# Performance work log

Hardware: AMD Instinct MI355X
Metric: run time of the kernel (lower is better)

## Reference

```python
import jax, jax.numpy as jnp
import numpy as np

B, N, D, E = 2, 50000, 128, 640000


def setup_inputs() -> dict:
    key = jax.random.key(0)
    ks = jax.random.split(key, 7)
    x = jax.random.normal(ks[0], (B, N, D), dtype=jnp.float32)
    edge_index = jax.random.randint(ks[1], (2, E), 0, N)
    edge_attr = jax.random.uniform(ks[2], (E,), dtype=jnp.float32)
    s = 1.0 / np.sqrt(D)
    W1 = jax.random.uniform(ks[3], (D, D), jnp.float32, -s, s)
    b1 = jax.random.uniform(ks[4], (D,), jnp.float32, -s, s)
    W2 = jax.random.uniform(ks[5], (D, D), jnp.float32, -s, s)
    b2 = jax.random.uniform(ks[6], (D,), jnp.float32, -s, s)
    return {"x": x, "edge_index": edge_index, "edge_attr": edge_attr,
            "W1": W1, "b1": b1, "W2": W2, "b2": b2}


def _gcn_layer(x, W, b, row, col, norm, n):
    # x: [B, N, D] -> transform then gather-scale-scatter along edges
    h = jnp.einsum('bnd,df->bnf', x, W)
    msg = h[:, row, :] * norm[None, :, None]          # [B, E2, D]
    agg = jax.vmap(lambda m: jax.ops.segment_sum(m, col, num_segments=n))(msg)
    return agg + b


def reference(x, edge_index, edge_attr, W1, b1, W2, b2):
    n = x.shape[1]
    row, col = edge_index[0], edge_index[1]
    # GCNConv default: add self loops (weight 1), symmetric normalization
    loop = jnp.arange(n)
    row2 = jnp.concatenate([row, loop])
    col2 = jnp.concatenate([col, loop])
    w2 = jnp.concatenate([edge_attr, jnp.ones((n,), edge_attr.dtype)])
    deg = jax.ops.segment_sum(w2, col2, num_segments=n)
    dinv = jnp.where(deg > 0, jax.lax.rsqrt(deg), 0.0)
    norm = dinv[row2] * w2 * dinv[col2]               # [E2]
    # dropout is identity in eval mode
    h = jax.nn.relu(_gcn_layer(x, W1, b1, row2, col2, norm, n))
    h = jax.nn.relu(_gcn_layer(h, W2, b2, row2, col2, norm, n))
    return h
```

## Files before the change

### kernel.cpp

```cpp
#include <hip/hip_runtime.h>

#define NNODES 50000
#define NBATCH 2
#define DIM    128
#define NEDGE  640000
#define M_TOT  (NBATCH*NNODES)
#define NXCD   8
#define NBL_N  196

typedef unsigned short u16;
typedef unsigned int   u32;
typedef unsigned long long u64;

typedef __attribute__((ext_vector_type(8))) short bf16x8;
typedef __attribute__((ext_vector_type(4))) float f32x4;

__device__ __forceinline__ float bf2f(u16 u){ return __uint_as_float(((u32)u)<<16); }
__device__ __forceinline__ u16 f2bf(float f){
    u32 x = __float_as_uint(f);
    x += 0x7fffu + ((x>>16)&1u);
    return (u16)(x>>16);
}

__global__ __launch_bounds__(256) void count_k(const int* __restrict__ ei,
                                               const float* __restrict__ ea,
                                               u64* __restrict__ part,
                                               u32* __restrict__ rankpack){
    u32 xcc = __builtin_amdgcn_s_getreg(6164) & 7u;
    int e = blockIdx.x*256 + threadIdx.x;
    if (e < NEDGE){
        int c = ei[NEDGE + e];
        u64 inc = (((u64)__float2uint_rn(ea[e] * 16777216.0f)) << 32) | 1ull;
        u64 old = __hip_atomic_fetch_add(&part[(size_t)xcc*NNODES + c], inc,
                                         __ATOMIC_RELAXED, __HIP_MEMORY_SCOPE_WORKGROUP);
        rankpack[e] = ((u32)old & 0xffffu) | (xcc << 16);
    }
}

__global__ __launch_bounds__(256) void scan1(const u64* __restrict__ part,
                                             int* __restrict__ cnt,
                                             int* __restrict__ poff,
                                             float* __restrict__ dinv,
                                             int* colstart, int* bsum){
    __shared__ int s[256];
    int tid = threadIdx.x;
    int n = blockIdx.x*256 + tid;
    int v = 0;
    if (n < NNODES){
        int run = 0; u64 fsum = 0;
        #pragma unroll
        for (int p = 0; p < NXCD; ++p){
            u64 pv = part[(size_t)p*NNODES + n];
            poff[p*NNODES + n] = run;
            run  += (int)(pv & 0xffffffffu);
            fsum += (pv >> 32);
        }
        cnt[n] = run;
        v = run;
        float deg = 1.0f + (float)fsum * (1.0f/16777216.0f);
        dinv[n] = rsqrtf(deg);
    }
    s[tid] = v; __syncthreads();
    #pragma unroll
    for (int off = 1; off < 256; off <<= 1){
        int t = (tid >= off) ? s[tid-off] : 0;
        __syncthreads();
        s[tid] += t;
        __syncthreads();
    }
    if (n < NNODES) colstart[n] = s[tid] - v;
    if (tid == 255) bsum[blockIdx.x] = s[255];
}

__global__ __launch_bounds__(256) void fill_k(const int* __restrict__ ei,
                                              const float* __restrict__ ea,
                                              const float* __restrict__ dinv,
                                              const int* __restrict__ colstart,
                                              const int* __restrict__ bsum,
                                              const int* __restrict__ poff,
                                              const u32* __restrict__ rankpack,
                                              int* __restrict__ colstartF,
                                              u32* __restrict__ epk){
    __shared__ int s[256];
    __shared__ int pre[256];
    int tid = threadIdx.x;
    int v = (tid < NBL_N) ? bsum[tid] : 0;
    s[tid] = v; __syncthreads();
    #pragma unroll
    for (int off = 1; off < 256; off <<= 1){
        int t = (tid >= off) ? s[tid-off] : 0;
        __syncthreads();
        s[tid] += t;
        __syncthreads();
    }
    pre[tid] = s[tid] - v;
    __syncthreads();

    int e = blockIdx.x*256 + tid;
    if (e < NEDGE){
        int r = ei[e], c = ei[NEDGE + e];
        u32 rp = rankpack[e];
        int base = colstart[c] + pre[c >> 8];
        colstartF[c] = base;
        int pos = base + poff[(rp >> 16)*NNODES + c] + (int)(rp & 0xffffu);
        float w = dinv[r] * ea[e] * dinv[c];
        epk[pos] = (u32)r | ((u32)f2bf(w) << 16);
    }
}

__global__ __launch_bounds__(256) void transposeW(const float* __restrict__ W1, u16* __restrict__ Wt1,
                                                  const float* __restrict__ W2, u16* __restrict__ Wt2,
                                                  u64* __restrict__ part){
    int i = blockIdx.x*256 + threadIdx.x;
    const float* W = (i < 16384) ? W1 : W2;
    u16* Wt       = (i < 16384) ? Wt1 : Wt2;
    int ii = i & 16383;
    int k = ii >> 7, n = ii & 127;
    Wt[n*DIM + k] = f2bf(W[ii]);
    for (int z = i; z < NXCD*NNODES; z += 32768) part[z] = 0;
}

__device__ __forceinline__ bf16x8 load_frag(const float* A, size_t off){
    const f32x4* ap = (const f32x4*)(A + off);
    f32x4 lo = __builtin_nontemporal_load(ap);
    f32x4 hi = __builtin_nontemporal_load(ap + 1);
    bf16x8 r;
    r[0] = (short)f2bf(lo.x); r[1] = (short)f2bf(lo.y);
    r[2] = (short)f2bf(lo.z); r[3] = (short)f2bf(lo.w);
    r[4] = (short)f2bf(hi.x); r[5] = (short)f2bf(hi.y);
    r[6] = (short)f2bf(hi.z); r[7] = (short)f2bf(hi.w);
    return r;
}
__device__ __forceinline__ bf16x8 load_frag(const u16* A, size_t off){
    return *(const bf16x8*)(A + off);
}

template <typename AT, bool PERM>
__global__ __launch_bounds__(256, 4) void gemm128(const AT* __restrict__ A,
                                                  const u16* __restrict__ Wt,
                                                  u16* __restrict__ H, int M){
    __shared__ u16 Wl[128][136];
    int tid = threadIdx.x;
    {
        const uint4* src = (const uint4*)Wt;
        #pragma unroll
        for (int j = 0; j < 8; ++j){
            int g = tid + j*256;
            *(uint4*)&Wl[g >> 4][(g & 15)*8] = src[g];
        }
    }
    __syncthreads();

    int wave = tid >> 6, lane = tid & 63;
    int quad = lane >> 4, r = lane & 15;
    int row0 = blockIdx.x*128;
    int rbase = row0 + wave*32;

    f32x4 acc[2][8];
    #pragma unroll
    for (int mt = 0; mt < 2; ++mt)
        #pragma unroll
        for (int nt = 0; nt < 8; ++nt)
            acc[mt][nt] = (f32x4){0.f,0.f,0.f,0.f};

    #pragma unroll
    for (int ks = 0; ks < 4; ++ks){
        bf16x8 af[2];
        #pragma unroll
        for (int mt = 0; mt < 2; ++mt){
            int row = rbase + mt*16 + r;
            if (row < M)
                af[mt] = load_frag(A, (size_t)row*DIM + ks*32 + quad*8);
            else
                af[mt] = (bf16x8){0,0,0,0,0,0,0,0};
        }
        #pragma unroll
        for (int nt = 0; nt < 8; ++nt){
            bf16x8 bfr = *(const bf16x8*)&Wl[nt*16 + r][ks*32 + quad*8];
            #pragma unroll
            for (int mt = 0; mt < 2; ++mt)
                acc[mt][nt] = __builtin_amdgcn_mfma_f32_16x16x32_bf16(af[mt], bfr, acc[mt][nt], 0, 0, 0);
        }
    }

    __syncthreads();
    #pragma unroll
    for (int mt = 0; mt < 2; ++mt)
        #pragma unroll
        for (int nt = 0; nt < 8; ++nt)
            #pragma unroll
            for (int reg = 0; reg < 4; ++reg)
                Wl[wave*32 + mt*16 + quad*4 + reg][nt*16 + r] = f2bf(acc[mt][nt][reg]);
    __syncthreads();

    #pragma unroll
    for (int j = 0; j < 8; ++j){
        int g = tid + j*256;
        int rl = g >> 4, ch = g & 15;
        int row = row0 + rl;
        if (row < M){
            size_t hrow;
            if (PERM){
                int b = (row >= NNODES);
                hrow = (size_t)(2*(row - b*NNODES) + b);
            } else {
                hrow = (size_t)row;
            }
            *(uint4*)((char*)H + hrow*256 + ch*16) = *(const uint4*)&Wl[rl][ch*8];
        }
    }
}

template <bool OUT_F32>
__global__ __launch_bounds__(256) void gather6_k(const u16* __restrict__ Hi,
                                                 const u32* __restrict__ epk,
                                                 const int* __restrict__ colstartF,
                                                 const int* __restrict__ cnt,
                                                 const float* __restrict__ dinv,
                                                 const float* __restrict__ bias,
                                                 void* __restrict__ out){
    int wave = threadIdx.x >> 6, lane = threadIdx.x & 63;
    int n = blockIdx.x*4 + wave;
    if (n >= NNODES) return;
    const char* Hb = (const char*)Hi;

    float a0, a1, a2, a3;
    {
        uint2 sv = *(const uint2*)(Hb + (size_t)n*512 + lane*8);
        float dn = dinv[n], dn2 = dn*dn;
        a0 = dn2*__uint_as_float(sv.x << 16);
        a1 = dn2*__uint_as_float(sv.x & 0xffff0000u);
        a2 = dn2*__uint_as_float(sv.y << 16);
        a3 = dn2*__uint_as_float(sv.y & 0xffff0000u);
    }

    int s = colstartF[n], c = cnt[n];
    for (int base = 0; base < c; base += 64){
        int m = min(64, c - base);
        u32 em = 0;
        if (lane < m) em = epk[s + base + lane];
        for (int j = 0; j < m; j += 8){
            #pragma unroll
            for (int g = 0; g < 8; ++g){
                u32 me = __shfl(em, j + g);
                uint2 v = *(const uint2*)(Hb + (size_t)(me & 0xffffu)*512 + lane*8);
                float w = __uint_as_float(me & 0xffff0000u);
                a0 = fmaf(w, __uint_as_float(v.x << 16), a0);
                a1 = fmaf(w, __uint_as_float(v.x & 0xffff0000u), a1);
                a2 = fmaf(w, __uint_as_float(v.y << 16), a2);
                a3 = fmaf(w, __uint_as_float(v.y & 0xffff0000u), a3);
            }
        }
    }

    int sub = lane & 31, b = lane >> 5;
    float4 bb = ((const float4*)bias)[sub];
    a0 = fmaxf(a0 + bb.x, 0.f);
    a1 = fmaxf(a1 + bb.y, 0.f);
    a2 = fmaxf(a2 + bb.z, 0.f);
    a3 = fmaxf(a3 + bb.w, 0.f);
    if (OUT_F32){
        float* O = (float*)out + ((size_t)b*NNODES + n)*DIM + sub*4;
        *(float4*)O = make_float4(a0, a1, a2, a3);
    } else {
        char* O = (char*)out + (size_t)n*512 + lane*8;
        uint2 pk;
        pk.x = (u32)f2bf(a0) | ((u32)f2bf(a1) << 16);
        pk.y = (u32)f2bf(a2) | ((u32)f2bf(a3) << 16);
        *(uint2*)O = pk;
    }
}

extern "C" void kernel_launch(void* const* d_in, const int* in_sizes, int n_in,
                              void* d_out, int out_size, void* d_ws, size_t ws_size,
                              hipStream_t stream){
    const float* x  = (const float*)d_in[0];
    const int*   ei = (const int*)  d_in[1];
    const float* ea = (const float*)d_in[2];
    const float* W1 = (const float*)d_in[3];
    const float* b1 = (const float*)d_in[4];
    const float* W2 = (const float*)d_in[5];
    const float* b2 = (const float*)d_in[6];

    char* p = (char*)d_ws;
    auto alloc = [&](size_t bytes)->char*{ char* r = p; p += (bytes + 511) & ~(size_t)511; return r; };
    u64*   part     = (u64*)  alloc((size_t)NXCD*NNODES*8);
    u32*   rankpack = (u32*)  alloc((size_t)NEDGE*4);
    int*   poff     = (int*)  alloc((size_t)NXCD*NNODES*4);
    float* dinv     = (float*)alloc(NNODES*4);
    int*   cnt      = (int*)  alloc(NNODES*4);
    int*   colstart = (int*)  alloc(NNODES*4);
    int*   colstartF= (int*)  alloc(NNODES*4);
    int*   bsum     = (int*)  alloc(1024);
    u32*   epk      = (u32*)  alloc((size_t)NEDGE*4);
    u16*   Wt1      = (u16*)  alloc(DIM*DIM*2);
    u16*   Wt2      = (u16*)  alloc(DIM*DIM*2);
    u16*   h        = (u16*)  alloc((size_t)M_TOT*DIM*2);
    u16*   o1       = (u16*)  alloc((size_t)M_TOT*DIM*2);

    const int NBL_E = (NEDGE  + 255)/256;
    const int NTILE = (M_TOT + 127)/128;
    const int NBL_G = (NNODES + 3)/4;

    transposeW<<<128, 256, 0, stream>>>(W1, Wt1, W2, Wt2, part);
    count_k<<<NBL_E, 256, 0, stream>>>(ei, ea, part, rankpack);
    scan1  <<<NBL_N, 256, 0, stream>>>(part, cnt, poff, dinv, colstart, bsum);
    fill_k <<<NBL_E, 256, 0, stream>>>(ei, ea, dinv, colstart, bsum, poff, rankpack, colstartF, epk);

    gemm128<float, true ><<<NTILE, 256, 0, stream>>>(x,  Wt1, h, M_TOT);
    gather6_k<false><<<NBL_G, 256, 0, stream>>>(h,  epk, colstartF, cnt, dinv, b1, o1);
    gemm128<u16,   false><<<NTILE, 256, 0, stream>>>(o1, Wt2, h, M_TOT);
    gather6_k<true ><<<NBL_G, 256, 0, stream>>>(h,  epk, colstartF, cnt, dinv, b2, d_out);
}
```

Before: 287.0 us.

## Store H batch-major and gather per batch with half-wave per node

```diff
diff --git a/kernel.cpp b/kernel.cpp
--- a/kernel.cpp
+++ b/kernel.cpp
@@ -7,6 +7,7 @@
 #define M_TOT  (NBATCH*NNODES)
 #define NXCD   8
 #define NBL_N  196
+#define NBL_GB 6250
 
 typedef unsigned short u16;
 typedef unsigned int   u32;
@@ -135,7 +136,7 @@
     return *(const bf16x8*)(A + off);
 }
 
-template <typename AT, bool PERM>
+template <typename AT>
 __global__ __launch_bounds__(256, 4) void gemm128(const AT* __restrict__ A,
                                                   const u16* __restrict__ Wt,
                                                   u16* __restrict__ H, int M){
@@ -198,21 +199,13 @@
         int g = tid + j*256;
         int rl = g >> 4, ch = g & 15;
         int row = row0 + rl;
-        if (row < M){
-            size_t hrow;
-            if (PERM){
-                int b = (row >= NNODES);
-                hrow = (size_t)(2*(row - b*NNODES) + b);
-            } else {
-                hrow = (size_t)row;
-            }
-            *(uint4*)((char*)H + hrow*256 + ch*16) = *(const uint4*)&Wl[rl][ch*8];
-        }
+        if (row < M)
+            *(uint4*)((char*)H + (size_t)row*256 + ch*16) = *(const uint4*)&Wl[rl][ch*8];
     }
 }
 
 template <bool OUT_F32>
-__global__ __launch_bounds__(256) void gather6_k(const u16* __restrict__ Hi,
+__global__ __launch_bounds__(256) void gather8_k(const u16* __restrict__ H,
                                                  const u32* __restrict__ epk,
                                                  const int* __restrict__ colstartF,
                                                  const int* __restrict__ cnt,
@@ -220,13 +213,15 @@
                                                  const float* __restrict__ bias,
                                                  void* __restrict__ out){
     int wave = threadIdx.x >> 6, lane = threadIdx.x & 63;
-    int n = blockIdx.x*4 + wave;
-    if (n >= NNODES) return;
-    const char* Hb = (const char*)Hi;
+    int sub = lane & 31, half = lane >> 5;
+    int bid = blockIdx.x;
+    int b   = (bid >= NBL_GB);
+    int n   = (bid - b*NBL_GB)*8 + wave*2 + half;
+    const char* Hb = (const char*)(H + (size_t)b*NNODES*DIM);
 
     float a0, a1, a2, a3;
     {
-        uint2 sv = *(const uint2*)(Hb + (size_t)n*512 + lane*8);
+        uint2 sv = *(const uint2*)(Hb + (size_t)n*256 + sub*8);
         float dn = dinv[n], dn2 = dn*dn;
         a0 = dn2*__uint_as_float(sv.x << 16);
         a1 = dn2*__uint_as_float(sv.x & 0xffff0000u);
@@ -235,15 +230,15 @@
     }
 
     int s = colstartF[n], c = cnt[n];
-    for (int base = 0; base < c; base += 64){
-        int m = min(64, c - base);
+    for (int base = 0; base < c; base += 32){
+        int m = min(32, c - base);
         u32 em = 0;
-        if (lane < m) em = epk[s + base + lane];
+        if (sub < m) em = epk[s + base + sub];
         for (int j = 0; j < m; j += 8){
             #pragma unroll
             for (int g = 0; g < 8; ++g){
-                u32 me = __shfl(em, j + g);
-                uint2 v = *(const uint2*)(Hb + (size_t)(me & 0xffffu)*512 + lane*8);
+                u32 me = __shfl(em, half*32 + j + g);
+                uint2 v = *(const uint2*)(Hb + (size_t)(me & 0xffffu)*256 + sub*8);
                 float w = __uint_as_float(me & 0xffff0000u);
                 a0 = fmaf(w, __uint_as_float(v.x << 16), a0);
                 a1 = fmaf(w, __uint_as_float(v.x & 0xffff0000u), a1);
@@ -253,7 +248,6 @@
         }
     }
 
-    int sub = lane & 31, b = lane >> 5;
     float4 bb = ((const float4*)bias)[sub];
     a0 = fmaxf(a0 + bb.x, 0.f);
     a1 = fmaxf(a1 + bb.y, 0.f);
@@ -263,7 +257,7 @@
         float* O = (float*)out + ((size_t)b*NNODES + n)*DIM + sub*4;
         *(float4*)O = make_float4(a0, a1, a2, a3);
     } else {
-        char* O = (char*)out + (size_t)n*512 + lane*8;
+        char* O = (char*)out + ((size_t)b*NNODES + n)*256 + sub*8;
         uint2 pk;
         pk.x = (u32)f2bf(a0) | ((u32)f2bf(a1) << 16);
         pk.y = (u32)f2bf(a2) | ((u32)f2bf(a3) << 16);
@@ -300,15 +294,15 @@
 
     const int NBL_E = (NEDGE  + 255)/256;
     const int NTILE = (M_TOT + 127)/128;
-    const int NBL_G = (NNODES + 3)/4;
+    const int NBL_G = 2*NBL_GB;
 
     transposeW<<<128, 256, 0, stream>>>(W1, Wt1, W2, Wt2, part);
     count_k<<<NBL_E, 256, 0, stream>>>(ei, ea, part, rankpack);
     scan1  <<<NBL_N, 256, 0, stream>>>(part, cnt, poff, dinv, colstart, bsum);
     fill_k <<<NBL_E, 256, 0, stream>>>(ei, ea, dinv, colstart, bsum, poff, rankpack, colstartF, epk);
 
-    gemm128<float, true ><<<NTILE, 256, 0, stream>>>(x,  Wt1, h, M_TOT);
-    gather6_k<false><<<NBL_G, 256, 0, stream>>>(h,  epk, colstartF, cnt, dinv, b1, o1);
-    gemm128<u16,   false><<<NTILE, 256, 0, stream>>>(o1, Wt2, h, M_TOT);
-    gather6_k<true ><<<NBL_G, 256, 0, stream>>>(h,  epk, colstartF, cnt, dinv, b2, d_out);
-}
+    gemm128<float><<<NTILE, 256, 0, stream>>>(x,  Wt1, h, M_TOT);
+    gather8_k<false><<<NBL_G, 256, 0, stream>>>(h,  epk, colstartF, cnt, dinv, b1, o1);
+    gemm128<u16  ><<<NTILE, 256, 0, stream>>>(o1, Wt2, h, M_TOT);
+    gather8_k<true ><<<NBL_G, 256, 0, stream>>>(h,  epk, colstartF, cnt, dinv, b2, d_out);
+}
```

Result: faster. 278.1 us, median of 2 (-3.1%).
